# Kernel tuning notes

Measured on AMD Instinct MI355X. Metric: run time of the kernel, lower is better.

The kernel has to match this reference:

```python
import jax, jax.numpy as jnp
import numpy as np

N = 100000   # nodes
F = 256      # input features
H = 64       # hidden dims
C = 40       # classes
L = 4        # GGNN layers
E = 1200000  # edges


def setup_inputs() -> dict:
    key = jax.random.key(0)
    ks = jax.random.split(key, 8)
    x = jax.random.normal(ks[0], (N, F), dtype=jnp.float32)
    edge_index = jax.random.randint(ks[1], (2, E), 0, N, dtype=jnp.int64)
    # glorot-initialized projection weights
    weight_in = jax.random.uniform(ks[2], (F, H), jnp.float32, -1.0, 1.0) * np.sqrt(6.0 / (F + H))
    weight_out = jax.random.uniform(ks[3], (H, C), jnp.float32, -1.0, 1.0) * np.sqrt(6.0 / (H + C))
    # GatedGraphConv: per-layer message weight [L, H, H], shared GRUCell params
    conv_weight = jax.random.uniform(ks[4], (L, H, H), jnp.float32, -1.0, 1.0) * np.sqrt(6.0 / (2 * H))
    s = 1.0 / np.sqrt(H)
    w_ih = jax.random.uniform(ks[5], (3 * H, H), jnp.float32, -s, s)
    w_hh = jax.random.uniform(ks[6], (3 * H, H), jnp.float32, -s, s)
    b_ih = jax.random.uniform(ks[7], (3 * H,), jnp.float32, -s, s)
    b_hh = jnp.zeros((3 * H,), jnp.float32)
    return {"x": x, "edge_index": edge_index, "weight_in": weight_in,
            "weight_out": weight_out, "conv_weight": conv_weight,
            "w_ih": w_ih, "w_hh": w_hh, "b_ih": b_ih, "b_hh": b_hh}


def _gru_cell(a, h, w_ih, w_hh, b_ih, b_hh):
    # torch.nn.GRUCell math: input a, hidden h
    gi = a @ w_ih.T + b_ih
    gh = h @ w_hh.T + b_hh
    i_r, i_z, i_n = jnp.split(gi, 3, axis=1)
    h_r, h_z, h_n = jnp.split(gh, 3, axis=1)
    r = jax.nn.sigmoid(i_r + h_r)
    z = jax.nn.sigmoid(i_z + h_z)
    n = jnp.tanh(i_n + r * h_n)
    return (1.0 - z) * n + z * h


def reference(x, edge_index, weight_in, weight_out, conv_weight, w_ih, w_hh, b_ih, b_hh):
    n_nodes = x.shape[0]
    src, dst = edge_index[0], edge_index[1]
    h = x @ weight_in  # [N, H]
    for i in range(conv_weight.shape[0]):
        m = h @ conv_weight[i]                                   # [N, H]
        agg = jax.ops.segment_sum(m[src], dst, num_segments=n_nodes)  # scatter-add
        h = _gru_cell(agg, h, w_ih, w_hh, b_ih, b_hh)
    out = h @ weight_out  # [N, C]
    return jax.nn.log_softmax(out, axis=1)
```

## Files before the change

### kernel.cpp

```cpp
#include <hip/hip_runtime.h>


#define DEVI __device__ __forceinline__

typedef __attribute__((ext_vector_type(8))) short short8;
typedef __attribute__((ext_vector_type(4))) short bf16x4;
typedef __attribute__((ext_vector_type(4))) float f32x4;

constexpr int N_NODES   = 100000;
constexpr int F_IN      = 256;
constexpr int H_DIM     = 64;
constexpr int C_OUT     = 40;
constexpr int ROW_TILES = N_NODES / 16;
constexpr int CH        = 8192;
constexpr int NBUCK     = (N_NODES + 127) / 128;
constexpr int LB_STRIDE = NBUCK + 1;
constexpr int BCAP      = 2048;
constexpr int LPAD      = 72;

DEVI float bf2f(unsigned short u) {
    unsigned v = ((unsigned)u) << 16;
    float f; __builtin_memcpy(&f, &v, 4); return f;
}
DEVI unsigned short f2bf(float f) {
    unsigned u; __builtin_memcpy(&u, &f, 4);
    unsigned r = u + 0x7FFFu + ((u >> 16) & 1u);
    return (unsigned short)(r >> 16);
}
DEVI float in_elem(const void* p, size_t idx, int f32flag) {
    return f32flag ? ((const float*)p)[idx]
                   : bf2f(((const unsigned short*)p)[idx]);
}
DEVI short8 f32row_to_frag(const float* __restrict__ p) {
    const f32x4* q = (const f32x4*)p;
    f32x4 lo = q[0], hi = q[1];
    short8 a;
    a[0] = (short)f2bf(lo[0]); a[1] = (short)f2bf(lo[1]);
    a[2] = (short)f2bf(lo[2]); a[3] = (short)f2bf(lo[3]);
    a[4] = (short)f2bf(hi[0]); a[5] = (short)f2bf(hi[1]);
    a[6] = (short)f2bf(hi[2]); a[7] = (short)f2bf(hi[3]);
    return a;
}

DEVI int probe_i64_wave(const int* __restrict__ ei) {
    int lane = threadIdx.x & 63;
    unsigned long long m = __ballot(ei[2 * lane + 1] == 0);
    return __popcll(m) >= 63;
}
DEVI int probe_f32_wave(const void* __restrict__ x) {
    const unsigned short* u = (const unsigned short*)x;
    int lane = threadIdx.x & 63;
    int cnt = 0;
#pragma unroll
    for (int i = 0; i < 4; ++i) {
        int e = (u[lane + i * 64] >> 7) & 0xFF;
        cnt += (e >= 100 && e <= 145) ? 1 : 0;
    }
#pragma unroll
    for (int d = 1; d < 64; d <<= 1) cnt += __shfl_xor(cnt, d);
    return cnt < 230;
}

__global__ __launch_bounds__(256) void bucket_local(
        const int* __restrict__ ei, int E, const void* __restrict__ x,
        int* __restrict__ wgsorted,
        int* __restrict__ lbase_g,
        int* __restrict__ flags) {
    __shared__ int hist[NBUCK];
    __shared__ int partial[256];
    __shared__ int staging[CH];
    int tid = threadIdx.x, wg = blockIdx.x;
    int i64 = probe_i64_wave(ei);
    if (wg == 0 && tid < 64) {
        int f32 = probe_f32_wave(x);
        if (tid == 0) { flags[0] = f32; flags[1] = i64; }
    }
    int base = wg * CH;
    int cnt_wg = min(CH, E - base);

    for (int i = tid; i < NBUCK; i += 256) hist[i] = 0;
    __syncthreads();
    for (int k = tid; k < cnt_wg; k += 256) {
        size_t e = (size_t)base + k;
        int d = i64 ? ei[2 * ((size_t)E + e)] : ei[(size_t)E + e];
        atomicAdd(&hist[d >> 7], 1);
    }
    __syncthreads();
    int i0 = 4 * tid;
    int e0 = (i0 + 0 < NBUCK) ? hist[i0 + 0] : 0;
    int e1 = (i0 + 1 < NBUCK) ? hist[i0 + 1] : 0;
    int e2 = (i0 + 2 < NBUCK) ? hist[i0 + 2] : 0;
    int e3 = (i0 + 3 < NBUCK) ? hist[i0 + 3] : 0;
    int s0 = e0, s1 = s0 + e1, s2 = s1 + e2, s3 = s2 + e3;
    __syncthreads();
    partial[tid] = s3;
    __syncthreads();
    for (int ofs = 1; ofs < 256; ofs <<= 1) {
        int add = (tid >= ofs) ? partial[tid - ofs] : 0;
        __syncthreads();
        partial[tid] += add;
        __syncthreads();
    }
    int pbase = (tid > 0) ? partial[tid - 1] : 0;
    if (i0 + 0 < NBUCK) hist[i0 + 0] = pbase;
    if (i0 + 1 < NBUCK) hist[i0 + 1] = pbase + s0;
    if (i0 + 2 < NBUCK) hist[i0 + 2] = pbase + s1;
    if (i0 + 3 < NBUCK) hist[i0 + 3] = pbase + s2;
    __syncthreads();
    int* lb = lbase_g + (size_t)wg * LB_STRIDE;
    for (int i = tid; i < NBUCK; i += 256) lb[i] = hist[i];
    if (tid == 0) lb[NBUCK] = cnt_wg;
    __syncthreads();
    for (int k = tid; k < cnt_wg; k += 256) {
        size_t e = (size_t)base + k;
        int s, d;
        if (i64) { s = ei[2 * e]; d = ei[2 * ((size_t)E + e)]; }
        else     { s = ei[e];     d = ei[(size_t)E + e]; }
        int pos = atomicAdd(&hist[d >> 7], 1);
        staging[pos] = ((d & 127) << 17) | s;
    }
    __syncthreads();
    for (int k = tid; k < cnt_wg; k += 256)
        wgsorted[(size_t)base + k] = staging[k];
}

__global__ __launch_bounds__(256) void bucket_csr_prep(
        const int* __restrict__ wgsorted,
        const int* __restrict__ lbase_g,
        int nwg,
        int* __restrict__ rowptr,
        int* __restrict__ counts,
        int* __restrict__ esrc,
        const void* __restrict__ w_in,
        const void* __restrict__ w_out,
        const void* __restrict__ w_hh,
        const void* __restrict__ b_ih,
        const void* __restrict__ b_hh,
        const void* __restrict__ conv_w,
        const void* __restrict__ w_ih,
        unsigned short* __restrict__ winfrag,
        unsigned short* __restrict__ wofrag,
        unsigned short* __restrict__ whh_c,
        unsigned short* __restrict__ bias_c,
        unsigned short* __restrict__ wcomb,
        const int* __restrict__ flags) {
    int tid = threadIdx.x, b = blockIdx.x;

    {
        int f32 = flags[0];
        int t = b * 256 + tid;
        if (t < 16384) {
            int i = t & 7, lane = (t >> 3) & 63, jt = (t >> 9) & 3, kb = t >> 11;
            int k = kb * 32 + ((lane >> 4) << 3) + i;
            int col = jt * 16 + (lane & 15);
            winfrag[t] = f2bf(in_elem(w_in, (size_t)k * 64 + col, f32));
        } else if (t < 19456) {
            int u = t - 16384;
            int i = u & 7, lane = (u >> 3) & 63;
            int jt = (u >> 9) % 3, kb = u / 1536;
            int k = kb * 32 + ((lane >> 4) << 3) + i;
            int col = jt * 16 + (lane & 15);
            wofrag[u] = (col < 40) ? f2bf(in_elem(w_out, (size_t)k * 40 + col, f32))
                                   : (unsigned short)0;
        } else if (t < 31744) {
            int u = t - 19456;
            whh_c[u] = f2bf(in_elem(w_hh, u, f32));
        } else if (t < 31936) {
            int u = t - 31744;
            bias_c[u] = f2bf(in_elem(b_ih, u, f32));
        } else if (t < 32128) {
            int u = t - 31936;
            bias_c[192 + u] = f2bf(in_elem(b_hh, u, f32));
        } else if (t < 32128 + 49152) {
            int u = t - 32128;
            int l = u / 12288;
            int idx = u % 12288;
            int i = idx & 7, lane = (idx >> 3) & 63, c = idx >> 9;
            int kb = c / 12, jt = c % 12;
            int quad = lane >> 4, l15 = lane & 15;
            int k = kb * 32 + quad * 8 + i;
            int g = jt * 16 + l15;
            float acc = 0.0f;
            if (f32) {
                const f32x4* ca = (const f32x4*)((const float*)conv_w +
                                                 (size_t)l * 4096 + (size_t)k * 64);
                const f32x4* wa = (const f32x4*)((const float*)w_ih + (size_t)g * 64);
#pragma unroll
                for (int jq = 0; jq < 16; ++jq) {
                    f32x4 cv = ca[jq];
                    f32x4 wv = wa[jq];
                    acc += cv[0] * wv[0] + cv[1] * wv[1] + cv[2] * wv[2] + cv[3] * wv[3];
                }
            } else {
                const short8* ca = (const short8*)((const unsigned short*)conv_w +
                                                   (size_t)l * 4096 + (size_t)k * 64);
                const short8* wa = (const short8*)((const unsigned short*)w_ih +
                                                   (size_t)g * 64);
#pragma unroll
                for (int jq = 0; jq < 8; ++jq) {
                    short8 cv = ca[jq];
                    short8 wv = wa[jq];
#pragma unroll
                    for (int q = 0; q < 8; ++q)
                        acc += bf2f((unsigned short)cv[q]) * bf2f((unsigned short)wv[q]);
                }
            }
            wcomb[(size_t)l * 12288 + idx] = f2bf(acc);
        }
    }

    __shared__ int segincl[256];
    __shared__ int segbase[256];
    __shared__ int edata[BCAP];
    __shared__ int sout[BCAP];
    __shared__ int hist2[128];
    __shared__ int cur2[128];

    int lbv = 0, cntv = 0;
    if (tid < nwg) {
        const int* lb = lbase_g + (size_t)tid * LB_STRIDE;
        lbv  = lb[b];
        cntv = lb[b + 1] - lbv;
    }
    segbase[tid] = lbv;
    segincl[tid] = cntv;
    __syncthreads();
    for (int ofs = 1; ofs < 256; ofs <<= 1) {
        int add = (tid >= ofs) ? segincl[tid - ofs] : 0;
        __syncthreads();
        segincl[tid] += add;
        __syncthreads();
    }
    int tot = min(segincl[255], BCAP);
    for (int i = tid; i < tot; i += 256) {
        int lo = 0, hi = 255;
        while (lo < hi) {
            int mid = (lo + hi) >> 1;
            if (segincl[mid] > i) hi = mid; else lo = mid + 1;
        }
        int excl = (lo > 0) ? segincl[lo - 1] : 0;
        edata[i] = wgsorted[(size_t)lo * CH + segbase[lo] + (i - excl)];
    }
    if (tid < 128) hist2[tid] = 0;
    __syncthreads();
    for (int i = tid; i < tot; i += 256) atomicAdd(&hist2[edata[i] >> 17], 1);
    __syncthreads();
    if (tid < 128) cur2[tid] = hist2[tid];
    __syncthreads();
    for (int ofs = 1; ofs < 128; ofs <<= 1) {
        int add = 0;
        if (tid < 128 && tid >= ofs) add = cur2[tid - ofs];
        __syncthreads();
        if (tid < 128) cur2[tid] += add;
        __syncthreads();
    }
    int nodeexcl = 0;
    if (tid < 128) nodeexcl = (tid > 0) ? cur2[tid - 1] : 0;
    __syncthreads();
    if (tid < 128) {
        int node = b * 128 + tid;
        if (node < N_NODES) {
            counts[node] = hist2[tid];
            rowptr[node] = b * BCAP + nodeexcl;
        }
        cur2[tid] = nodeexcl;
    }
    __syncthreads();
    for (int i = tid; i < tot; i += 256) {
        int p = edata[i];
        int pos = atomicAdd(&cur2[p >> 17], 1);
        sout[pos] = p & 0x1FFFF;
    }
    __syncthreads();
    for (int i = tid; i < tot; i += 256)
        esrc[(size_t)b * BCAP + i] = sout[i];
}

template <int XF32>
DEVI void proj_in_body(const void* __restrict__ xr,
                       const unsigned short* __restrict__ wfrag,
                       unsigned short* __restrict__ h) {
    int wid = blockIdx.x * 4 + (threadIdx.x >> 6);
    if (wid >= ROW_TILES) return;
    int lane = threadIdx.x & 63;
    int l15 = lane & 15, quad = lane >> 4;
    int row0 = wid * 16;
    int arow = row0 + l15;

    f32x4 acc[4];
#pragma unroll
    for (int jt = 0; jt < 4; ++jt) acc[jt] = (f32x4)(0.0f);

#pragma unroll
    for (int kb = 0; kb < 8; ++kb) {
        short8 a;
        if (XF32)
            a = f32row_to_frag((const float*)xr + (size_t)arow * F_IN + kb * 32 + quad * 8);
        else
            a = *(const short8*)((const unsigned short*)xr + (size_t)arow * F_IN + kb * 32 + quad * 8);
#pragma unroll
        for (int jt = 0; jt < 4; ++jt) {
            short8 b = *(const short8*)(wfrag + (size_t)((kb * 4 + jt) * 64 + lane) * 8);
            acc[jt] = __builtin_amdgcn_mfma_f32_16x16x32_bf16(a, b, acc[jt], 0, 0, 0);
        }
    }
#pragma unroll
    for (int jt = 0; jt < 4; ++jt)
#pragma unroll
        for (int r = 0; r < 4; ++r)
            h[(size_t)(row0 + quad * 4 + r) * H_DIM + jt * 16 + l15] = f2bf(acc[jt][r]);
}

__global__ __launch_bounds__(256) void proj_in_kernel(
        const void* __restrict__ x,
        const unsigned short* __restrict__ wfrag,
        unsigned short* __restrict__ h,
        const int* __restrict__ flags) {
    if (flags[0]) proj_in_body<1>(x, wfrag, h);
    else          proj_in_body<0>(x, wfrag, h);
}

template <int LAST>
__global__ __launch_bounds__(256, 6) void layer_fused(
        const unsigned short* __restrict__ hin,
        unsigned short* __restrict__ hout,
        const int* __restrict__ rowptr,
        const int* __restrict__ counts,
        const int* __restrict__ esrc,
        const unsigned short* __restrict__ wcomb_l,
        const unsigned short* __restrict__ whh_c,
        const unsigned short* __restrict__ bias_c,
        const unsigned short* __restrict__ wofrag,
        void* __restrict__ out,
        const int* __restrict__ flags) {
    __shared__ __align__(16) unsigned short lagg[64 * LPAD];
    int tid = threadIdx.x;
    int w = tid >> 6, lane = tid & 63;
    int nb0 = blockIdx.x * 64;
    int sub = lane >> 4;
    int c4 = (lane & 15) * 4;

    for (int k = 0; k < 16; ++k) {
        int n = nb0 + w * 16 + k;
        if (n >= N_NODES) break;
        int start = rowptr[n];
        int deg   = counts[n];
        f32x4 acc0 = (f32x4)(0.0f), acc1 = (f32x4)(0.0f);
        for (int i = 0; i < deg; i += 32) {
            int sidx[8];
#pragma unroll
            for (int u = 0; u < 8; ++u) {
                int e = i + u * 4 + sub;
                sidx[u] = (e < deg) ? esrc[start + e] : -1;
            }
#pragma unroll
            for (int u = 0; u < 8; ++u) {
                if (sidx[u] >= 0) {
                    bf16x4 v = *(const bf16x4*)(hin + (size_t)sidx[u] * H_DIM + c4);
                    f32x4& A = (u & 1) ? acc1 : acc0;
                    A[0] += bf2f((unsigned short)v[0]);
                    A[1] += bf2f((unsigned short)v[1]);
                    A[2] += bf2f((unsigned short)v[2]);
                    A[3] += bf2f((unsigned short)v[3]);
                }
            }
        }
#pragma unroll
        for (int q = 0; q < 4; ++q) acc0[q] += acc1[q];
#pragma unroll
        for (int q = 0; q < 4; ++q) {
            acc0[q] += __shfl_xor(acc0[q], 16);
            acc0[q] += __shfl_xor(acc0[q], 32);
        }
        if (sub == 0) {
            bf16x4 o;
            o[0] = (short)f2bf(acc0[0]);
            o[1] = (short)f2bf(acc0[1]);
            o[2] = (short)f2bf(acc0[2]);
            o[3] = (short)f2bf(acc0[3]);
            *(bf16x4*)(lagg + (w * 16 + k) * LPAD + c4) = o;
        }
    }
    __syncthreads();

    int l15 = lane & 15, quad = lane >> 4;
    int row0 = nb0 + w * 16;
    int lrow = w * 16 + l15;
    int arow = min(row0 + l15, N_NODES - 1);

    short8 aa0 = *(const short8*)(lagg + lrow * LPAD + quad * 8);
    short8 aa1 = *(const short8*)(lagg + lrow * LPAD + 32 + quad * 8);
    short8 ah0 = *(const short8*)(hin + (size_t)arow * H_DIM + quad * 8);
    short8 ah1 = *(const short8*)(hin + (size_t)arow * H_DIM + 32 + quad * 8);

#pragma unroll 1
    for (int jc = 0; jc < 4; ++jc) {
        f32x4 ir = (f32x4)(0.0f), iz = (f32x4)(0.0f), ia = (f32x4)(0.0f);
        f32x4 hr = (f32x4)(0.0f), hz = (f32x4)(0.0f), ha = (f32x4)(0.0f);
#define WCF(kb, jt) (*(const short8*)(wcomb_l + (size_t)(((kb) * 12 + (jt)) * 64 + lane) * 8))
#define WHF(jt, kb) (*(const short8*)(whh_c + (size_t)((jt) * 16 + l15) * H_DIM + (kb) * 32 + quad * 8))
        ir = __builtin_amdgcn_mfma_f32_16x16x32_bf16(aa0, WCF(0, jc), ir, 0, 0, 0);
        iz = __builtin_amdgcn_mfma_f32_16x16x32_bf16(aa0, WCF(0, 4 + jc), iz, 0, 0, 0);
        ia = __builtin_amdgcn_mfma_f32_16x16x32_bf16(aa0, WCF(0, 8 + jc), ia, 0, 0, 0);
        hr = __builtin_amdgcn_mfma_f32_16x16x32_bf16(ah0, WHF(jc, 0), hr, 0, 0, 0);
        hz = __builtin_amdgcn_mfma_f32_16x16x32_bf16(ah0, WHF(4 + jc, 0), hz, 0, 0, 0);
        ha = __builtin_amdgcn_mfma_f32_16x16x32_bf16(ah0, WHF(8 + jc, 0), ha, 0, 0, 0);
        ir = __builtin_amdgcn_mfma_f32_16x16x32_bf16(aa1, WCF(1, jc), ir, 0, 0, 0);
        iz = __builtin_amdgcn_mfma_f32_16x16x32_bf16(aa1, WCF(1, 4 + jc), iz, 0, 0, 0);
        ia = __builtin_amdgcn_mfma_f32_16x16x32_bf16(aa1, WCF(1, 8 + jc), ia, 0, 0, 0);
        hr = __builtin_amdgcn_mfma_f32_16x16x32_bf16(ah1, WHF(jc, 1), hr, 0, 0, 0);
        hz = __builtin_amdgcn_mfma_f32_16x16x32_bf16(ah1, WHF(4 + jc, 1), hz, 0, 0, 0);
        ha = __builtin_amdgcn_mfma_f32_16x16x32_bf16(ah1, WHF(8 + jc, 1), ha, 0, 0, 0);
#undef WCF
#undef WHF
        int j = jc * 16 + l15;
        float bir = bf2f(bias_c[j]),       bhr = bf2f(bias_c[192 + j]);
        float biz = bf2f(bias_c[64 + j]),  bhz = bf2f(bias_c[256 + j]);
        float bin = bf2f(bias_c[128 + j]), bhn = bf2f(bias_c[320 + j]);
#pragma unroll
        for (int r = 0; r < 4; ++r) {
            int row = row0 + quad * 4 + r;
            if (row < N_NODES) {
                float xr = (ir[r] + bir) + (hr[r] + bhr);
                float xz = (iz[r] + biz) + (hz[r] + bhz);
                float in_ = ia[r] + bin;
                float hn_ = ha[r] + bhn;
                xr = fminf(fmaxf(xr, -30.0f), 30.0f);
                xz = fminf(fmaxf(xz, -30.0f), 30.0f);
                float rg = 1.0f / (1.0f + __expf(-xr));
                float zg = 1.0f / (1.0f + __expf(-xz));
                float na = in_ + rg * hn_;
                float ey = __expf(-2.0f * fabsf(na));
                float th = (1.0f - ey) / (1.0f + ey);
                float nt = (na < 0.0f) ? -th : th;
                float ho = bf2f(hin[(size_t)row * H_DIM + j]);
                hout[(size_t)row * H_DIM + j] = f2bf((1.0f - zg) * nt + zg * ho);
            }
        }
    }

    if (LAST) {
        int f32out = flags[0];
        f32x4 pacc[3];
#pragma unroll
        for (int jt = 0; jt < 3; ++jt) pacc[jt] = (f32x4)(0.0f);
#pragma unroll
        for (int kb = 0; kb < 2; ++kb) {
            short8 a = *(const short8*)(hout + (size_t)arow * H_DIM + kb * 32 + quad * 8);
#pragma unroll
            for (int jt = 0; jt < 3; ++jt) {
                short8 bfr = *(const short8*)(wofrag + (size_t)((kb * 3 + jt) * 64 + lane) * 8);
                pacc[jt] = __builtin_amdgcn_mfma_f32_16x16x32_bf16(a, bfr, pacc[jt], 0, 0, 0);
            }
        }
        float* of = (float*)out;
        unsigned short* ob = (unsigned short*)out;
        bool valid2 = (l15 < 8);
#pragma unroll
        for (int r = 0; r < 4; ++r) {
            int row = row0 + quad * 4 + r;
            float v0 = pacc[0][r], v1 = pacc[1][r], v2 = pacc[2][r];
            float mx = fmaxf(v0, v1);
            if (valid2) mx = fmaxf(mx, v2);
#pragma unroll
            for (int d = 1; d < 16; d <<= 1) mx = fmaxf(mx, __shfl_xor(mx, d));
            float s = __expf(v0 - mx) + __expf(v1 - mx) + (valid2 ? __expf(v2 - mx) : 0.0f);
#pragma unroll
            for (int d = 1; d < 16; d <<= 1) s += __shfl_xor(s, d);
            float lg = mx + __logf(s);
            if (row < N_NODES) {
                size_t o0 = (size_t)row * C_OUT + l15;
                if (f32out) {
                    of[o0]      = v0 - lg;
                    of[o0 + 16] = v1 - lg;
                    if (valid2) of[o0 + 32] = v2 - lg;
                } else {
                    ob[o0]      = f2bf(v0 - lg);
                    ob[o0 + 16] = f2bf(v1 - lg);
                    if (valid2) ob[o0 + 32] = f2bf(v2 - lg);
                }
            }
        }
    }
}

extern "C" void kernel_launch(void* const* d_in, const int* in_sizes, int n_in,
                              void* d_out, int out_size, void* d_ws, size_t ws_size,
                              hipStream_t stream) {
    const void* x      = d_in[0];
    const int*  ei     = (const int*)d_in[1];
    const void* w_in   = d_in[2];
    const void* w_out  = d_in[3];
    const void* conv_w = d_in[4];
    const void* w_ih   = d_in[5];
    const void* w_hh   = d_in[6];
    const void* b_ih   = d_in[7];
    const void* b_hh   = d_in[8];

    const int E   = in_sizes[1] / 2;
    const int nwg = (E + CH - 1) / CH;

    char* ws = (char*)d_ws;
    size_t off = 0;
    auto carve = [&](size_t bytes) {
        void* p = ws + off;
        off += (bytes + 255) & ~(size_t)255;
        return p;
    };
    int*            flags    = (int*)carve(256);
    unsigned short* h1       = (unsigned short*)carve((size_t)N_NODES * H_DIM * 2);
    unsigned short* h0       = (unsigned short*)carve((size_t)N_NODES * H_DIM * 2);
    int*            counts   = (int*)carve((size_t)N_NODES * 4);
    int*            rowptr   = (int*)carve((size_t)N_NODES * 4);
    int*            wgsorted = (int*)carve((size_t)nwg * CH * 4);
    int*            lbase_g  = (int*)carve((size_t)nwg * LB_STRIDE * 4);
    int*            esrcP    = (int*)carve((size_t)NBUCK * BCAP * 4);
    unsigned short* winfrag  = (unsigned short*)carve((size_t)16384 * 2);
    unsigned short* wcomb    = (unsigned short*)carve((size_t)4 * 12288 * 2);
    unsigned short* wofrag   = (unsigned short*)carve((size_t)3072 * 2);
    unsigned short* whh_c    = (unsigned short*)carve((size_t)12288 * 2);
    unsigned short* bias_c   = (unsigned short*)carve((size_t)384 * 2);

    bucket_local<<<nwg, 256, 0, stream>>>(ei, E, x, wgsorted, lbase_g, flags);
    bucket_csr_prep<<<NBUCK, 256, 0, stream>>>(
        wgsorted, lbase_g, nwg, rowptr, counts, esrcP,
        w_in, w_out, w_hh, b_ih, b_hh, conv_w, w_ih,
        winfrag, wofrag, whh_c, bias_c, wcomb, flags);

    const int gblocks = (ROW_TILES + 3) / 4;

    proj_in_kernel<<<gblocks, 256, 0, stream>>>(x, winfrag, h0, flags);

    layer_fused<0><<<gblocks, 256, 0, stream>>>(h0, h1, rowptr, counts, esrcP,
        wcomb + 0 * 12288, whh_c, bias_c, wofrag, d_out, flags);
    layer_fused<0><<<gblocks, 256, 0, stream>>>(h1, h0, rowptr, counts, esrcP,
        wcomb + 1 * 12288, whh_c, bias_c, wofrag, d_out, flags);
    layer_fused<0><<<gblocks, 256, 0, stream>>>(h0, h1, rowptr, counts, esrcP,
        wcomb + 2 * 12288, whh_c, bias_c, wofrag, d_out, flags);
    layer_fused<1><<<gblocks, 256, 0, stream>>>(h1, h0, rowptr, counts, esrcP,
        wcomb + 3 * 12288, whh_c, bias_c, wofrag, d_out, flags);
}
```

Baseline: 640.5 us.

## Shrink layer blocks to 16 nodes and split GRU output columns across waves

Each layer block now handles 16 nodes instead of 64. Each wave aggregates 4 nodes, then each of the 4 waves computes one 16-column chunk of the GRU output instead of looping over all four chunks. The grid grows fourfold, which is meant to improve load balance across irregular node degrees and raise parallelism in the GEMM/GRU phase. The last layer stages the new hidden state in LDS and wave 0 computes the output projection and log-softmax, so h is no longer reread from global memory. In exchange, every wave redundantly loads the A fragments, and weight fragment reads increase per node.

```diff
diff --git a/kernel.cpp b/kernel.cpp
--- a/kernel.cpp
+++ b/kernel.cpp
@@ -333,16 +333,17 @@
         const unsigned short* __restrict__ wofrag,
         void* __restrict__ out,
         const int* __restrict__ flags) {
-    __shared__ __align__(16) unsigned short lagg[64 * LPAD];
+    __shared__ __align__(16) unsigned short lagg[16 * LPAD];
+    __shared__ __align__(16) unsigned short hnew[16 * LPAD];
     int tid = threadIdx.x;
     int w = tid >> 6, lane = tid & 63;
-    int nb0 = blockIdx.x * 64;
+    int nb0 = blockIdx.x * 16;
     int sub = lane >> 4;
     int c4 = (lane & 15) * 4;
 
-    for (int k = 0; k < 16; ++k) {
-        int n = nb0 + w * 16 + k;
-        if (n >= N_NODES) break;
+#pragma unroll 1
+    for (int k = 0; k < 4; ++k) {
+        int n = nb0 + w * 4 + k;
         int start = rowptr[n];
         int deg   = counts[n];
         f32x4 acc0 = (f32x4)(0.0f), acc1 = (f32x4)(0.0f);
@@ -378,23 +379,21 @@
             o[1] = (short)f2bf(acc0[1]);
             o[2] = (short)f2bf(acc0[2]);
             o[3] = (short)f2bf(acc0[3]);
-            *(bf16x4*)(lagg + (w * 16 + k) * LPAD + c4) = o;
+            *(bf16x4*)(lagg + (w * 4 + k) * LPAD + c4) = o;
         }
     }
     __syncthreads();
 
     int l15 = lane & 15, quad = lane >> 4;
-    int row0 = nb0 + w * 16;
-    int lrow = w * 16 + l15;
-    int arow = min(row0 + l15, N_NODES - 1);
-
-    short8 aa0 = *(const short8*)(lagg + lrow * LPAD + quad * 8);
-    short8 aa1 = *(const short8*)(lagg + lrow * LPAD + 32 + quad * 8);
+    int arow = nb0 + l15;
+    int jc = w;
+
+    short8 aa0 = *(const short8*)(lagg + l15 * LPAD + quad * 8);
+    short8 aa1 = *(const short8*)(lagg + l15 * LPAD + 32 + quad * 8);
     short8 ah0 = *(const short8*)(hin + (size_t)arow * H_DIM + quad * 8);
     short8 ah1 = *(const short8*)(hin + (size_t)arow * H_DIM + 32 + quad * 8);
 
-#pragma unroll 1
-    for (int jc = 0; jc < 4; ++jc) {
+    {
         f32x4 ir = (f32x4)(0.0f), iz = (f32x4)(0.0f), ia = (f32x4)(0.0f);
         f32x4 hr = (f32x4)(0.0f), hz = (f32x4)(0.0f), ha = (f32x4)(0.0f);
 #define WCF(kb, jt) (*(const short8*)(wcomb_l + (size_t)(((kb) * 12 + (jt)) * 64 + lane) * 8))
@@ -419,56 +418,57 @@
         float bin = bf2f(bias_c[128 + j]), bhn = bf2f(bias_c[320 + j]);
 #pragma unroll
         for (int r = 0; r < 4; ++r) {
-            int row = row0 + quad * 4 + r;
-            if (row < N_NODES) {
-                float xr = (ir[r] + bir) + (hr[r] + bhr);
-                float xz = (iz[r] + biz) + (hz[r] + bhz);
-                float in_ = ia[r] + bin;
-                float hn_ = ha[r] + bhn;
-                xr = fminf(fmaxf(xr, -30.0f), 30.0f);
-                xz = fminf(fmaxf(xz, -30.0f), 30.0f);
-                float rg = 1.0f / (1.0f + __expf(-xr));
-                float zg = 1.0f / (1.0f + __expf(-xz));
-                float na = in_ + rg * hn_;
-                float ey = __expf(-2.0f * fabsf(na));
-                float th = (1.0f - ey) / (1.0f + ey);
-                float nt = (na < 0.0f) ? -th : th;
-                float ho = bf2f(hin[(size_t)row * H_DIM + j]);
-                hout[(size_t)row * H_DIM + j] = f2bf((1.0f - zg) * nt + zg * ho);
+            int row = nb0 + quad * 4 + r;
+            float xr = (ir[r] + bir) + (hr[r] + bhr);
+            float xz = (iz[r] + biz) + (hz[r] + bhz);
+            float in_ = ia[r] + bin;
+            float hn_ = ha[r] + bhn;
+            xr = fminf(fmaxf(xr, -30.0f), 30.0f);
+            xz = fminf(fmaxf(xz, -30.0f), 30.0f);
+            float rg = 1.0f / (1.0f + __expf(-xr));
+            float zg = 1.0f / (1.0f + __expf(-xz));
+            float na = in_ + rg * hn_;
+            float ey = __expf(-2.0f * fabsf(na));
+            float th = (1.0f - ey) / (1.0f + ey);
+            float nt = (na < 0.0f) ? -th : th;
+            float ho = bf2f(hin[(size_t)row * H_DIM + j]);
+            unsigned short hv = f2bf((1.0f - zg) * nt + zg * ho);
+            if (LAST) hnew[(quad * 4 + r) * LPAD + j] = hv;
+            else      hout[(size_t)row * H_DIM + j] = hv;
+        }
+    }
+
+    if (LAST) {
+        __syncthreads();
+        if (w == 0) {
+            int f32out = flags[0];
+            f32x4 pacc[3];
+#pragma unroll
+            for (int jt = 0; jt < 3; ++jt) pacc[jt] = (f32x4)(0.0f);
+#pragma unroll
+            for (int kb = 0; kb < 2; ++kb) {
+                short8 a = *(const short8*)(hnew + l15 * LPAD + kb * 32 + quad * 8);
+#pragma unroll
+                for (int jt = 0; jt < 3; ++jt) {
+                    short8 bfr = *(const short8*)(wofrag + (size_t)((kb * 3 + jt) * 64 + lane) * 8);
+                    pacc[jt] = __builtin_amdgcn_mfma_f32_16x16x32_bf16(a, bfr, pacc[jt], 0, 0, 0);
+                }
             }
-        }
-    }
-
-    if (LAST) {
-        int f32out = flags[0];
-        f32x4 pacc[3];
-#pragma unroll
-        for (int jt = 0; jt < 3; ++jt) pacc[jt] = (f32x4)(0.0f);
-#pragma unroll
-        for (int kb = 0; kb < 2; ++kb) {
-            short8 a = *(const short8*)(hout + (size_t)arow * H_DIM + kb * 32 + quad * 8);
-#pragma unroll
-            for (int jt = 0; jt < 3; ++jt) {
-                short8 bfr = *(const short8*)(wofrag + (size_t)((kb * 3 + jt) * 64 + lane) * 8);
-                pacc[jt] = __builtin_amdgcn_mfma_f32_16x16x32_bf16(a, bfr, pacc[jt], 0, 0, 0);
-            }
-        }
-        float* of = (float*)out;
-        unsigned short* ob = (unsigned short*)out;
-        bool valid2 = (l15 < 8);
-#pragma unroll
-        for (int r = 0; r < 4; ++r) {
-            int row = row0 + quad * 4 + r;
-            float v0 = pacc[0][r], v1 = pacc[1][r], v2 = pacc[2][r];
-            float mx = fmaxf(v0, v1);
-            if (valid2) mx = fmaxf(mx, v2);
-#pragma unroll
-            for (int d = 1; d < 16; d <<= 1) mx = fmaxf(mx, __shfl_xor(mx, d));
-            float s = __expf(v0 - mx) + __expf(v1 - mx) + (valid2 ? __expf(v2 - mx) : 0.0f);
-#pragma unroll
-            for (int d = 1; d < 16; d <<= 1) s += __shfl_xor(s, d);
-            float lg = mx + __logf(s);
-            if (row < N_NODES) {
+            float* of = (float*)out;
+            unsigned short* ob = (unsigned short*)out;
+            bool valid2 = (l15 < 8);
+#pragma unroll
+            for (int r = 0; r < 4; ++r) {
+                int row = nb0 + quad * 4 + r;
+                float v0 = pacc[0][r], v1 = pacc[1][r], v2 = pacc[2][r];
+                float mx = fmaxf(v0, v1);
+                if (valid2) mx = fmaxf(mx, v2);
+#pragma unroll
+                for (int d = 1; d < 16; d <<= 1) mx = fmaxf(mx, __shfl_xor(mx, d));
+                float s = __expf(v0 - mx) + __expf(v1 - mx) + (valid2 ? __expf(v2 - mx) : 0.0f);
+#pragma unroll
+                for (int d = 1; d < 16; d <<= 1) s += __shfl_xor(s, d);
+                float lg = mx + __logf(s);
                 size_t o0 = (size_t)row * C_OUT + l15;
                 if (f32out) {
                     of[o0]      = v0 - lg;
@@ -528,15 +528,16 @@
         winfrag, wofrag, whh_c, bias_c, wcomb, flags);
 
     const int gblocks = (ROW_TILES + 3) / 4;
+    const int lblocks = N_NODES / 16;
 
     proj_in_kernel<<<gblocks, 256, 0, stream>>>(x, winfrag, h0, flags);
 
-    layer_fused<0><<<gblocks, 256, 0, stream>>>(h0, h1, rowptr, counts, esrcP,
+    layer_fused<0><<<lblocks, 256, 0, stream>>>(h0, h1, rowptr, counts, esrcP,
         wcomb + 0 * 12288, whh_c, bias_c, wofrag, d_out, flags);
-    layer_fused<0><<<gblocks, 256, 0, stream>>>(h1, h0, rowptr, counts, esrcP,
+    layer_fused<0><<<lblocks, 256, 0, stream>>>(h1, h0, rowptr, counts, esrcP,
         wcomb + 1 * 12288, whh_c, bias_c, wofrag, d_out, flags);
-    layer_fused<0><<<gblocks, 256, 0, stream>>>(h0, h1, rowptr, counts, esrcP,
+    layer_fused<0><<<lblocks, 256, 0, stream>>>(h0, h1, rowptr, counts, esrcP,
         wcomb + 2 * 12288, whh_c, bias_c, wofrag, d_out, flags);
-    layer_fused<1><<<gblocks, 256, 0, stream>>>(h1, h0, rowptr, counts, esrcP,
+    layer_fused<1><<<lblocks, 256, 0, stream>>>(h1, h0, rowptr, counts, esrcP,
         wcomb + 3 * 12288, whh_c, bias_c, wofrag, d_out, flags);
 }
```

After: 544.2 us. 15.0% less time.
